# Optimization experiments

Hardware: AMD Instinct MI355X
Metric: run time of the kernel (lower is better)

Reference implementation:

```python
import jax, jax.numpy as jnp
import numpy as np

B, NP, NV, E = 256, 500, 50, 128
FP, FV = 16, 16
DEG_P, DEG_V = 6, 4


def setup_inputs() -> dict:
    key = jax.random.key(0)
    ks = jax.random.split(key, 16)
    rng = np.random.default_rng(0)

    def edges(nb, n, deg):
        per = deg * n
        off = np.repeat(np.arange(nb, dtype=np.int32) * n, per)
        ei = off[None, :] + rng.integers(0, n, size=(2, nb * per)).astype(np.int32)
        return jnp.asarray(ei)

    inp = {
        "p_x": jax.random.normal(ks[0], (B * NP, FP), jnp.float32),
        "v_x": jax.random.normal(ks[1], (B * NV, FV), jnp.float32),
        "p_edge_index": edges(B, NP, DEG_P),
        "v_edge_index": edges(B, NV, DEG_V),
        "p_batch": jnp.asarray(np.repeat(np.arange(B, dtype=np.int32), NP)),
        "v_batch": jnp.asarray(np.repeat(np.arange(B, dtype=np.int32), NV)),
    }

    def lin(k, fi, fo):
        s = 1.0 / np.sqrt(fi)
        kw, kb = jax.random.split(k)
        return (jax.random.uniform(kw, (fi, fo), jnp.float32, -s, s),
                jax.random.uniform(kb, (fo,), jnp.float32, -s, s))

    layers = [("pW0", "pb0", FP, E), ("pW1", "pb1", E, E), ("pW2", "pb2", E, E),
              ("vW0", "vb0", FV, E), ("vW1", "vb1", E, E), ("vW2", "vb2", E, E),
              ("hW1", "hb1", 4 * E, 2 * E), ("hW2", "hb2", 2 * E, E), ("hW3", "hb3", E, 1)]
    for j, (wn, bn, fi, fo) in enumerate(layers):
        W, b = lin(ks[2 + j], fi, fo)
        inp[wn] = W
        inp[bn] = b
    return inp


def _gcn(h, src, dst, dinv, W, b):
    # GCNConv: out[i] = sum_{j->i} dinv[j]*dinv[i] * (h[j] @ W) + dinv[i]^2 * (h[i] @ W) + b
    xw = h @ W
    msg = xw[src] * (dinv[src] * dinv[dst])[:, None]
    agg = jax.ops.segment_sum(msg, dst, num_segments=h.shape[0])
    return agg + xw * (dinv * dinv)[:, None] + b


def _encoder(x, edge_index, batch, W0, b0, W1, b1, W2, b2, nb, npg):
    N = x.shape[0]
    src, dst = edge_index[0], edge_index[1]
    h0 = x @ W0 + b0                                   # node_init_embeddings [N, E]
    ones_e = jnp.ones(src.shape[0], x.dtype)
    deg = 1.0 + jax.ops.segment_sum(ones_e, dst, num_segments=N)  # includes self loop
    dinv = jax.lax.rsqrt(deg)
    h = jax.nn.relu(_gcn(h0, src, dst, dinv, W1, b1))
    h = _gcn(h, src, dst, dinv, W2, b2)                # node_embeddings [N, E]
    counts = jax.ops.segment_sum(jnp.ones(N, x.dtype), batch, num_segments=nb)
    graph = jax.ops.segment_sum(h, batch, num_segments=nb) / counts[:, None]  # [nb, E]
    hd = h.reshape(nb, npg, -1)                        # to_dense_batch (equal-size graphs)
    h0d = h0.reshape(nb, npg, -1)
    gr = jnp.broadcast_to(graph[:, None, :], hd.shape)
    concat = jnp.concatenate([hd, h0d, gr], axis=-1)   # [nb, npg, 3E]
    mask = jnp.ones((nb, npg), bool)
    return graph, concat, mask


def reference(p_x, v_x, p_edge_index, v_edge_index, p_batch, v_batch,
              pW0, pb0, pW1, pb1, pW2, pb2,
              vW0, vb0, vW1, vb1, vW2, vb2,
              hW1, hb1, hW2, hb2, hW3, hb3):
    p_graph, _, _ = _encoder(p_x, p_edge_index, p_batch, pW0, pb0, pW1, pb1, pW2, pb2, B, NP)
    _, v_concat, v_mask = _encoder(v_x, v_edge_index, v_batch, vW0, vb0, vW1, vb1, vW2, vb2, B, NV)
    pg_rep = jnp.broadcast_to(p_graph[:, None, :], (B, NV, p_graph.shape[-1]))
    x = jnp.concatenate([v_concat, pg_rep], axis=-1)   # [B, NV, 4E]
    h = jax.nn.leaky_relu(x @ hW1 + hb1)
    h = jax.nn.leaky_relu(h @ hW2 + hb2)
    logits = (h @ hW3 + hb3)[..., 0]                   # [B, NV]
    return jnp.where(v_mask, logits, jnp.float32(-1e9))
```

## Files before the change

kernel.cpp:

```cpp
#include <hip/hip_runtime.h>
#include <hip/hip_bf16.h>

#define NP_TOT 128000
#define NV_TOT 12800
#define EP_EDGES 768000
#define EV_EDGES 51200
#define NB 256
#define PEPG 3000
#define VEPG 200
#define VCAP 24
#define PITCHV 138

typedef short bf16x8 __attribute__((ext_vector_type(8)));
typedef float f32x4 __attribute__((ext_vector_type(4)));

static __device__ __forceinline__ unsigned short f2bf(float f) {
    unsigned u = __builtin_bit_cast(unsigned, f);
    unsigned r = u + 0x7FFFu + ((u >> 16) & 1u);
    return (unsigned short)(r >> 16);
}
static __device__ __forceinline__ float bf2f(unsigned short h) {
    return __builtin_bit_cast(float, (unsigned)h << 16);
}

static __device__ __forceinline__ void frag_elem(const float* __restrict__ W,
                                                 short* __restrict__ Fh,
                                                 short* __restrict__ Fl,
                                                 int K, int M, int e) {
    if (e >= K * M) return;
    int col = e % M, kk = e / M;
    int ks = kk >> 5, rem = kk & 31, fq = rem >> 3, j = rem & 7;
    float v = W[(size_t)kk * M + col];
    unsigned short h = f2bf(v);
    size_t dst = (((size_t)col * (K >> 5) + ks) * 4 + fq) * 8 + j;
    Fh[dst] = (short)h;
    Fl[dst] = (short)f2bf(v - bf2f(h));
}

__global__ __launch_bounds__(256) void prep_k(
    const float* __restrict__ pW0, const float* __restrict__ pb0,
    const float* __restrict__ pW1,
    float* __restrict__ W01, float* __restrict__ b01,
    const float* __restrict__ vW1, short* __restrict__ W1vh, short* __restrict__ W1vl,
    const float* __restrict__ vW2, short* __restrict__ W2vh, short* __restrict__ W2vl,
    const float* __restrict__ hW1, short* __restrict__ H1h, short* __restrict__ H1l,
    const float* __restrict__ hW2, short* __restrict__ H2h, short* __restrict__ H2l) {
    int bid = blockIdx.x, t = threadIdx.x;
    if (bid == 0) {
        if (t < 128) {
            int col = t;
            float acc[17];
            #pragma unroll
            for (int r = 0; r < 17; r++) acc[r] = 0.f;
            for (int i = 0; i < 128; i++) {
                float w1 = pW1[i * 128 + col];
                #pragma unroll
                for (int r = 0; r < 16; r++) acc[r] += pW0[r * 128 + i] * w1;
                acc[16] += pb0[i] * w1;
            }
            #pragma unroll
            for (int r = 0; r < 16; r++) W01[r * 128 + col] = acc[r];
            b01[col] = acc[16];
        }
    } else if (bid < 65) {
        frag_elem(vW1, W1vh, W1vl, 128, 128, (bid - 1) * 256 + t);
    } else if (bid < 129) {
        frag_elem(vW2, W2vh, W2vl, 128, 128, (bid - 65) * 256 + t);
    } else if (bid < 641) {
        frag_elem(hW1, H1h, H1l, 512, 256, (bid - 129) * 256 + t);
    } else {
        frag_elem(hW2, H2h, H2l, 256, 128, (bid - 641) * 256 + t);
    }
}

__global__ __launch_bounds__(512) void pfused3(const float* __restrict__ x,
                                               const int* __restrict__ ei,
                                               const float* __restrict__ W01,
                                               const float* __restrict__ b01,
                                               const float* __restrict__ b1,
                                               float* __restrict__ p_gz) {
    __shared__ char lds[77824];
    float* sx = (float*)lds;
    unsigned short* sadj = (unsigned short*)(lds + 34816);
    char*  zb    = lds + 59392;
    float* sdinv = (float*)(lds + 69632);
    int*   scnt  = (int*)(lds + 71680);
    float* sbeta = (float*)(lds + 73728);
    float* scsum = (float*)(lds + 75776);

    const int t = threadIdx.x;
    const int b = blockIdx.x;

    scnt[t] = 0; scsum[t] = 0.f;
    const float4* x4 = (const float4*)(x + (size_t)b * 500 * 16);
    for (int i = t; i < 2000; i += 512) {
        float4 v = x4[i];
        int n = i >> 2, q = i & 3;
        float* dst = &sx[n * 17 + q * 4];
        dst[0] = v.x; dst[1] = v.y; dst[2] = v.z; dst[3] = v.w;
    }
    __syncthreads();

    const int* esrc = ei + (size_t)b * PEPG;
    const int* edst = ei + EP_EDGES + (size_t)b * PEPG;
    const int base = b * 500;

    for (int e = t; e < PEPG; e += 512) {
        int s = esrc[e] - base, d = edst[e] - base;
        int slot = atomicAdd(&scnt[d], 1);
        if (slot < VCAP) sadj[d * VCAP + slot] = (unsigned short)s;
    }
    __syncthreads();
    sdinv[t] = rsqrtf(1.0f + (float)scnt[t]);
    __syncthreads();

    for (int e = t; e < PEPG; e += 512)
        atomicAdd(&scsum[esrc[e] - base], sdinv[edst[e] - base]);
    __syncthreads();
    scsum[t] = (t < 500) ? sdinv[t] * (sdinv[t] + scsum[t]) * (1.0f / 500.0f) : 0.f;

    const int lane = t & 63;
    const int wvi = t >> 6;
    const int fr = lane & 15;
    const int fq = lane >> 4;
    const int col = wvi * 16 + fr;
    bf16x8 B1, B2;
    {
        float wt[8];
        #pragma unroll
        for (int j = 0; j < 8; j++)
            wt[j] = W01[(size_t)((fq * 8 + j) & 15) * 128 + col];
        short b1a[8], b2a[8];
        #pragma unroll
        for (int j = 0; j < 8; j++) {
            int kk = fq * 8 + j;
            unsigned short h = f2bf(wt[j]);
            b1a[j] = (short)h;
            b2a[j] = (kk < 16) ? (short)f2bf(wt[j] - bf2f(h)) : (short)0;
        }
        B1 = (bf16x8){b1a[0],b1a[1],b1a[2],b1a[3],b1a[4],b1a[5],b1a[6],b1a[7]};
        B2 = (bf16x8){b2a[0],b2a[1],b2a[2],b2a[3],b2a[4],b2a[5],b2a[6],b2a[7]};
    }
    float b01c = b01[col];
    float b1c = b1[col];
    float pools = 0.f;

    const int cg = t & 7, nb_ = t >> 3, c0 = cg * 2;
    #pragma unroll
    for (int ch = 0; ch < 4; ch++) {
        __syncthreads();
        #pragma unroll
        for (int pass = 0; pass < 2; pass++) {
            int n = ch * 128 + pass * 64 + nb_;
            char* zr = zb + (pass * 64 + nb_) * 80 + cg * 4;
            if (n < 500) {
                float di = sdinv[n];
                int d = scnt[n]; if (d > VCAP) d = VCAP;
                const unsigned short* ap = sadj + n * VCAP;
                float a0 = 0.f, a1 = 0.f, ts = 0.f;
                for (int e = 0; e < d; e++) {
                    int jl = ap[e];
                    float dj = sdinv[jl];
                    a0 += dj * sx[jl * 17 + c0];
                    a1 += dj * sx[jl * 17 + c0 + 1];
                    ts += dj;
                }
                float z0 = di * (di * sx[n * 17 + c0] + a0);
                float z1 = di * (di * sx[n * 17 + c0 + 1] + a1);
                unsigned short h0 = f2bf(z0), h1 = f2bf(z1);
                unsigned short l0 = f2bf(z0 - bf2f(h0)), l1 = f2bf(z1 - bf2f(h1));
                *(unsigned*)(zr)      = (unsigned)h0 | ((unsigned)h1 << 16);
                *(unsigned*)(zr + 32) = (unsigned)l0 | ((unsigned)l1 << 16);
                if (cg == 0) sbeta[n] = di * (di + ts);
            } else {
                *(unsigned*)(zr) = 0u;
                *(unsigned*)(zr + 32) = 0u;
                if (cg == 0) sbeta[n] = 0.f;
            }
        }
        __syncthreads();
        f32x4 acc[8];
        #pragma unroll
        for (int m = 0; m < 8; m++) acc[m] = (f32x4){0.f, 0.f, 0.f, 0.f};
        #pragma unroll
        for (int m = 0; m < 8; m++) {
            int rl = m * 16 + fr;
            bf16x8 a = *(bf16x8*)(zb + rl * 80 + fq * 16);
            acc[m] = __builtin_amdgcn_mfma_f32_16x16x32_bf16(a, B1, acc[m], 0, 0, 0);
            acc[m] = __builtin_amdgcn_mfma_f32_16x16x32_bf16(a, B2, acc[m], 0, 0, 0);
        }
        #pragma unroll
        for (int m = 0; m < 8; m++)
            #pragma unroll
            for (int j = 0; j < 4; j++) {
                int rl = ch * 128 + m * 16 + fq * 4 + j;
                float v = fmaxf(acc[m][j] + sbeta[rl] * b01c + b1c, 0.f);
                pools += scsum[rl] * v;
            }
    }
    pools += __shfl_xor(pools, 16);
    pools += __shfl_xor(pools, 32);
    if (fq == 0) p_gz[(size_t)b * 128 + col] = pools;
}

#define LB 0
#define LC 35328
#define LD 68096
#define LE 100864
#define E_SDINV (LE)
#define E_SCNT  (LE + 256)
#define E_SADJ  (LE + 512)
#define E_SVG   (LE + 5376)
#define E_VGH   (LE + 5888)
#define E_VGL   (LE + 6144)
#define E_PGH   (LE + 6400)
#define E_PGL   (LE + 6656)
#define E_WSUM  (LE + 6912)
__global__ __launch_bounds__(512) void vhead_k(
    const float* __restrict__ v_x,
    const int* __restrict__ v_ei,
    const float* __restrict__ W0, const float* __restrict__ b0,
    const short* __restrict__ W1h, const short* __restrict__ W1l,
    const float* __restrict__ b1,
    const short* __restrict__ W2h, const short* __restrict__ W2l,
    const float* __restrict__ b2,
    const float* __restrict__ p_gz,
    const float* __restrict__ pW2, const float* __restrict__ pb2,
    const short* __restrict__ H1h, const short* __restrict__ H1l,
    const float* __restrict__ hb1,
    const short* __restrict__ H2h, const short* __restrict__ H2l,
    const float* __restrict__ hb2,
    const float* __restrict__ w3, const float* __restrict__ b3,
    float* __restrict__ out) {
    __shared__ char lds[109824];
    const int t = threadIdx.x;
    const int b = blockIdx.x;
    const int lane = t & 63;
    const int wv = t >> 6;
    const int fr = lane & 15;
    const int fq = lane >> 4;
    float* Bf = (float*)(lds + LB);
    float* sdinv = (float*)(lds + E_SDINV);
    int*   scnt  = (int*)(lds + E_SCNT);
    int*   sadj  = (int*)(lds + E_SADJ);

    if (t < 64) scnt[t] = 0;
    *(float4*)(lds + LC + t * 16) = *((const float4*)W0 + t);
    {
        int col = t & 127, q = t >> 7;
        const float* gz = p_gz + (size_t)b * 128;
        float s = 0.f;
        #pragma unroll
        for (int k = 0; k < 32; k++)
            s += gz[q * 32 + k] * pW2[(size_t)(q * 32 + k) * 128 + col];
        ((float*)(lds + E_WSUM))[q * 128 + col] = s;
    }
    __syncthreads();

    if (t < VEPG) {
        int s = v_ei[b * VEPG + t] - b * 50;
        int d = v_ei[EV_EDGES + b * VEPG + t] - b * 50;
        int slot = atomicAdd(&scnt[d], 1);
        if (slot < VCAP) sadj[d * VCAP + slot] = s;
    }
    __syncthreads();

    if (t < 64)
        sdinv[t] = (t < 50) ? rsqrtf(1.0f + (float)scnt[t]) : 0.f;
    if (t < 128) {
        float* part = (float*)(lds + E_WSUM);
        float v = part[t] + part[128 + t] + part[256 + t] + part[384 + t] + pb2[t];
        unsigned short h = f2bf(v);
        ((short*)(lds + E_PGH))[t] = (short)h;
        ((short*)(lds + E_PGL))[t] = (short)f2bf(v - bf2f(h));
    }
    {
        int n = t >> 3, cg = t & 7;
        if (n < 50) {
            const float* sW0 = (const float*)(lds + LC);
            const float4* xr = (const float4*)(v_x + (size_t)(b * 50 + n) * 16);
            float4 x0 = xr[0], x1 = xr[1], x2 = xr[2], x3 = xr[3];
            float xv[16] = {x0.x,x0.y,x0.z,x0.w, x1.x,x1.y,x1.z,x1.w,
                            x2.x,x2.y,x2.z,x2.w, x3.x,x3.y,x3.z,x3.w};
            #pragma unroll
            for (int cc = 0; cc < 16; cc++) {
                int c = cg + cc * 8;
                float a = b0[c];
                #pragma unroll
                for (int k = 0; k < 16; k++) a += xv[k] * sW0[k * 128 + c];
                Bf[n * PITCHV + c] = a;
            }
        }
    }
    __syncthreads();

    {
        #pragma unroll
        for (int g = 0; g < 8; g++) {
            int r = g * 8 + wv;
            float2 v = *(const float2*)&Bf[r * PITCHV + 2 * lane];
            unsigned short h0 = f2bf(v.x), h1 = f2bf(v.y);
            unsigned short l0 = f2bf(v.x - bf2f(h0)), l1 = f2bf(v.y - bf2f(h1));
            int q = (256 + 4 * lane) ^ ((r & 7) << 4);
            *(unsigned*)(lds + LC + r * 512 + q) = (unsigned)h0 | ((unsigned)h1 << 16);
            *(unsigned*)(lds + LD + r * 512 + q) = (unsigned)l0 | ((unsigned)l1 << 16);
        }
        for (int g = 0; g < 7; g++) {
            int n = g * 8 + wv;
            if (n < 50) {
                float di = sdinv[n];
                int d = scnt[n]; if (d > VCAP) d = VCAP;
                const int* ap = sadj + n * VCAP;
                float2 a = *(const float2*)&Bf[n * PITCHV + 2 * lane];
                a.x *= di; a.y *= di;
                for (int e = 0; e < d; e++) {
                    int jl = ap[e];
                    float dj = sdinv[jl];
                    float2 v = *(const float2*)&Bf[jl * PITCHV + 2 * lane];
                    a.x += dj * v.x; a.y += dj * v.y;
                }
                float z0 = di * a.x, z1 = di * a.y;
                unsigned short h0 = f2bf(z0), h1 = f2bf(z1);
                unsigned short l0 = f2bf(z0 - bf2f(h0)), l1 = f2bf(z1 - bf2f(h1));
                int q = (4 * lane) ^ ((n & 7) << 4);
                *(unsigned*)(lds + LC + n * 512 + q) = (unsigned)h0 | ((unsigned)h1 << 16);
                *(unsigned*)(lds + LD + n * 512 + q) = (unsigned)l0 | ((unsigned)l1 << 16);
            }
        }
    }
    __syncthreads();

    {
        const int col = wv * 16 + fr;
        bf16x8 bh[4], bl[4];
        #pragma unroll
        for (int ks = 0; ks < 4; ks++) {
            int base = ((col * 4 + ks) * 4 + fq) * 8;
            bh[ks] = *(const bf16x8*)&W1h[base];
            bl[ks] = *(const bf16x8*)&W1l[base];
        }
        f32x4 acc[4];
        #pragma unroll
        for (int m = 0; m < 4; m++) acc[m] = (f32x4){0.f,0.f,0.f,0.f};
        #pragma unroll
        for (int ks = 0; ks < 4; ks++) {
            int kb = ks * 64 + fq * 16;
            #pragma unroll
            for (int m = 0; m < 4; m++) {
                int r = m * 16 + fr;
                int off = r * 512 + (kb ^ ((r & 7) << 4));
                bf16x8 ah = *(bf16x8*)(lds + LC + off);
                bf16x8 al = *(bf16x8*)(lds + LD + off);
                acc[m] = __builtin_amdgcn_mfma_f32_16x16x32_bf16(ah, bh[ks], acc[m], 0, 0, 0);
                acc[m] = __builtin_amdgcn_mfma_f32_16x16x32_bf16(ah, bl[ks], acc[m], 0, 0, 0);
                acc[m] = __builtin_amdgcn_mfma_f32_16x16x32_bf16(al, bh[ks], acc[m], 0, 0, 0);
            }
        }
        float b1c = b1[col];
        #pragma unroll
        for (int m = 0; m < 4; m++)
            #pragma unroll
            for (int j = 0; j < 4; j++) {
                int row = m * 16 + fq * 4 + j;
                Bf[row * PITCHV + col] = fmaxf(acc[m][j] + b1c, 0.f);
            }
    }
    __syncthreads();

    {
        for (int g = 0; g < 7; g++) {
            int n = g * 8 + wv;
            if (n < 50) {
                float di = sdinv[n];
                int d = scnt[n]; if (d > VCAP) d = VCAP;
                const int* ap = sadj + n * VCAP;
                float2 a = *(const float2*)&Bf[n * PITCHV + 2 * lane];
                a.x *= di; a.y *= di;
                for (int e = 0; e < d; e++) {
                    int jl = ap[e];
                    float dj = sdinv[jl];
                    float2 v = *(const float2*)&Bf[jl * PITCHV + 2 * lane];
                    a.x += dj * v.x; a.y += dj * v.y;
                }
                float z0 = di * a.x, z1 = di * a.y;
                unsigned short h0 = f2bf(z0), h1 = f2bf(z1);
                unsigned short l0 = f2bf(z0 - bf2f(h0)), l1 = f2bf(z1 - bf2f(h1));
                int q = (4 * lane) ^ ((n & 7) << 4);
                *(unsigned*)(lds + LC + n * 512 + q) = (unsigned)h0 | ((unsigned)h1 << 16);
                *(unsigned*)(lds + LD + n * 512 + q) = (unsigned)l0 | ((unsigned)l1 << 16);
            }
        }
    }
    __syncthreads();

    float h2v[4][4];
    {
        const int col = wv * 16 + fr;
        bf16x8 bh[4], bl[4];
        #pragma unroll
        for (int ks = 0; ks < 4; ks++) {
            int base = ((col * 4 + ks) * 4 + fq) * 8;
            bh[ks] = *(const bf16x8*)&W2h[base];
            bl[ks] = *(const bf16x8*)&W2l[base];
        }
        f32x4 acc[4];
        #pragma unroll
        for (int m = 0; m < 4; m++) acc[m] = (f32x4){0.f,0.f,0.f,0.f};
        #pragma unroll
        for (int ks = 0; ks < 4; ks++) {
            int kb = ks * 64 + fq * 16;
            #pragma unroll
            for (int m = 0; m < 4; m++) {
                int r = m * 16 + fr;
                int off = r * 512 + (kb ^ ((r & 7) << 4));
                bf16x8 ah = *(bf16x8*)(lds + LC + off);
                bf16x8 al = *(bf16x8*)(lds + LD + off);
                acc[m] = __builtin_amdgcn_mfma_f32_16x16x32_bf16(ah, bh[ks], acc[m], 0, 0, 0);
                acc[m] = __builtin_amdgcn_mfma_f32_16x16x32_bf16(ah, bl[ks], acc[m], 0, 0, 0);
                acc[m] = __builtin_amdgcn_mfma_f32_16x16x32_bf16(al, bh[ks], acc[m], 0, 0, 0);
            }
        }
        float b2c = b2[col];
        #pragma unroll
        for (int m = 0; m < 4; m++)
            #pragma unroll
            for (int j = 0; j < 4; j++) h2v[m][j] = acc[m][j] + b2c;
    }
    __syncthreads();

    {
        const int col = wv * 16 + fr;
        float s = 0.f;
        #pragma unroll
        for (int m = 0; m < 4; m++)
            #pragma unroll
            for (int j = 0; j < 4; j++) {
                int row = m * 16 + fq * 4 + j;
                float v = h2v[m][j];
                unsigned short h = f2bf(v);
                unsigned short l = f2bf(v - bf2f(h));
                int q = (2 * col) ^ ((row & 7) << 4);
                *(short*)(lds + LC + row * 512 + q) = (short)h;
                *(short*)(lds + LD + row * 512 + q) = (short)l;
                if (row < 50) s += v;
            }
        s += __shfl_xor(s, 16); s += __shfl_xor(s, 32);
        if (fq == 0) ((float*)(lds + E_SVG))[col] = s * (1.0f / 50.0f);
    }
    __syncthreads();

    if (t < 128) {
        float v = ((float*)(lds + E_SVG))[t];
        unsigned short h = f2bf(v);
        ((short*)(lds + E_VGH))[t] = (short)h;
        ((short*)(lds + E_VGL))[t] = (short)f2bf(v - bf2f(h));
    }
    __syncthreads();

    f32x4 accT[4][2];
    #pragma unroll
    for (int m = 0; m < 4; m++)
        #pragma unroll
        for (int nf = 0; nf < 2; nf++) accT[m][nf] = (f32x4){0.f,0.f,0.f,0.f};
    {
        #pragma unroll
        for (int ks = 0; ks < 16; ks++) {
            bf16x8 bh[2], bl[2];
            #pragma unroll
            for (int nf = 0; nf < 2; nf++) {
                int col2 = wv * 32 + nf * 16 + fr;
                int base = ((col2 * 16 + ks) * 4 + fq) * 8;
                bh[nf] = *(const bf16x8*)&H1h[base];
                bl[nf] = *(const bf16x8*)&H1l[base];
            }
            if (ks < 8) {
                int kb = ks * 64 + fq * 16;
                #pragma unroll
                for (int m = 0; m < 4; m++) {
                    int r = m * 16 + fr;
                    int off = r * 512 + (kb ^ ((r & 7) << 4));
                    bf16x8 ah = *(bf16x8*)(lds + LC + off);
                    bf16x8 al = *(bf16x8*)(lds + LD + off);
                    #pragma unroll
                    for (int nf = 0; nf < 2; nf++) {
                        accT[m][nf] = __builtin_amdgcn_mfma_f32_16x16x32_bf16(ah, bh[nf], accT[m][nf], 0, 0, 0);
                        accT[m][nf] = __builtin_amdgcn_mfma_f32_16x16x32_bf16(ah, bl[nf], accT[m][nf], 0, 0, 0);
                        accT[m][nf] = __builtin_amdgcn_mfma_f32_16x16x32_bf16(al, bh[nf], accT[m][nf], 0, 0, 0);
                    }
                }
            } else {
                int boff = (ks < 12) ? (E_VGH + (ks - 8) * 64 + fq * 16)
                                     : (E_PGH + (ks - 12) * 64 + fq * 16);
                int loff = boff + 256;
                bf16x8 ah = *(bf16x8*)(lds + boff);
                bf16x8 al = *(bf16x8*)(lds + loff);
                #pragma unroll
                for (int m = 0; m < 4; m++)
                    #pragma unroll
                    for (int nf = 0; nf < 2; nf++) {
                        accT[m][nf] = __builtin_amdgcn_mfma_f32_16x16x32_bf16(ah, bh[nf], accT[m][nf], 0, 0, 0);
                        accT[m][nf] = __builtin_amdgcn_mfma_f32_16x16x32_bf16(ah, bl[nf], accT[m][nf], 0, 0, 0);
                        accT[m][nf] = __builtin_amdgcn_mfma_f32_16x16x32_bf16(al, bh[nf], accT[m][nf], 0, 0, 0);
                    }
            }
        }
    }
    __syncthreads();
    {
        #pragma unroll
        for (int nf = 0; nf < 2; nf++) {
            int col2 = wv * 32 + nf * 16 + fr;
            float hc = hb1[col2];
            #pragma unroll
            for (int m = 0; m < 4; m++)
                #pragma unroll
                for (int j = 0; j < 4; j++) {
                    int row = m * 16 + fq * 4 + j;
                    float v = accT[m][nf][j] + hc;
                    v = v > 0.f ? v : 0.01f * v;
                    unsigned short h = f2bf(v);
                    unsigned short l = f2bf(v - bf2f(h));
                    int q = (2 * col2) ^ ((row & 7) << 4);
                    *(short*)(lds + LC + row * 512 + q) = (short)h;
                    *(short*)(lds + LD + row * 512 + q) = (short)l;
                }
        }
    }
    __syncthreads();

    {
        const int col3 = wv * 16 + fr;
        f32x4 acc[4];
        #pragma unroll
        for (int m = 0; m < 4; m++) acc[m] = (f32x4){0.f,0.f,0.f,0.f};
        #pragma unroll
        for (int ks = 0; ks < 8; ks++) {
            int base = ((col3 * 8 + ks) * 4 + fq) * 8;
            bf16x8 bh = *(const bf16x8*)&H2h[base];
            bf16x8 bl = *(const bf16x8*)&H2l[base];
            int kb = ks * 64 + fq * 16;
            #pragma unroll
            for (int m = 0; m < 4; m++) {
                int r = m * 16 + fr;
                int off = r * 512 + (kb ^ ((r & 7) << 4));
                bf16x8 ah = *(bf16x8*)(lds + LC + off);
                bf16x8 al = *(bf16x8*)(lds + LD + off);
                acc[m] = __builtin_amdgcn_mfma_f32_16x16x32_bf16(ah, bh, acc[m], 0, 0, 0);
                acc[m] = __builtin_amdgcn_mfma_f32_16x16x32_bf16(ah, bl, acc[m], 0, 0, 0);
                acc[m] = __builtin_amdgcn_mfma_f32_16x16x32_bf16(al, bh, acc[m], 0, 0, 0);
            }
        }
        float hc = hb2[col3], wc = w3[col3];
        float p[4][4];
        #pragma unroll
        for (int m = 0; m < 4; m++)
            #pragma unroll
            for (int j = 0; j < 4; j++) {
                float v = acc[m][j] + hc;
                v = v > 0.f ? v : 0.01f * v;
                p[m][j] = v * wc;
            }
        #pragma unroll
        for (int m = 0; m < 4; m++)
            #pragma unroll
            for (int j = 0; j < 4; j++) {
                p[m][j] += __shfl_xor(p[m][j], 1);
                p[m][j] += __shfl_xor(p[m][j], 2);
                p[m][j] += __shfl_xor(p[m][j], 4);
                p[m][j] += __shfl_xor(p[m][j], 8);
            }
        if (fr == 0) {
            float* wsum = (float*)(lds + E_WSUM);
            #pragma unroll
            for (int m = 0; m < 4; m++)
                #pragma unroll
                for (int j = 0; j < 4; j++)
                    wsum[wv * 64 + m * 16 + fq * 4 + j] = p[m][j];
        }
    }
    __syncthreads();
    if (t < 50) {
        float* wsum = (float*)(lds + E_WSUM);
        float s = 0.f;
        #pragma unroll
        for (int w8 = 0; w8 < 8; w8++) s += wsum[w8 * 64 + t];
        out[b * 50 + t] = s + b3[0];
    }
}

extern "C" void kernel_launch(void* const* d_in, const int* in_sizes, int n_in,
                              void* d_out, int out_size, void* d_ws, size_t ws_size,
                              hipStream_t stream) {
    const float* p_x = (const float*)d_in[0];
    const float* v_x = (const float*)d_in[1];
    const int* p_ei = (const int*)d_in[2];
    const int* v_ei = (const int*)d_in[3];
    const float* pW0 = (const float*)d_in[6];  const float* pb0 = (const float*)d_in[7];
    const float* pW1 = (const float*)d_in[8];  const float* pb1 = (const float*)d_in[9];
    const float* pW2 = (const float*)d_in[10]; const float* pb2 = (const float*)d_in[11];
    const float* vW0 = (const float*)d_in[12]; const float* vb0 = (const float*)d_in[13];
    const float* vW1 = (const float*)d_in[14]; const float* vb1 = (const float*)d_in[15];
    const float* vW2 = (const float*)d_in[16]; const float* vb2 = (const float*)d_in[17];
    const float* hW1 = (const float*)d_in[18]; const float* hb1 = (const float*)d_in[19];
    const float* hW2 = (const float*)d_in[20]; const float* hb2 = (const float*)d_in[21];
    const float* hW3 = (const float*)d_in[22]; const float* hb3 = (const float*)d_in[23];

    char* w = (char*)d_ws;
    size_t off = 0;
    auto alloc = [&](size_t bytes) { char* p = w + off; off += (bytes + 255) & ~size_t(255); return p; };
    float* p_gz = (float*)alloc((size_t)NB * 128 * 4);
    float* W01  = (float*)alloc((size_t)16 * 128 * 4);
    float* b01  = (float*)alloc((size_t)128 * 4);
    short* W1vh = (short*)alloc((size_t)128 * 128 * 2);
    short* W1vl = (short*)alloc((size_t)128 * 128 * 2);
    short* W2vh = (short*)alloc((size_t)128 * 128 * 2);
    short* W2vl = (short*)alloc((size_t)128 * 128 * 2);
    short* H1h  = (short*)alloc((size_t)512 * 256 * 2);
    short* H1l  = (short*)alloc((size_t)512 * 256 * 2);
    short* H2h  = (short*)alloc((size_t)256 * 128 * 2);
    short* H2l  = (short*)alloc((size_t)256 * 128 * 2);

    prep_k<<<769, 256, 0, stream>>>(pW0, pb0, pW1, W01, b01,
                                    vW1, W1vh, W1vl, vW2, W2vh, W2vl,
                                    hW1, H1h, H1l, hW2, H2h, H2l);
    pfused3<<<NB, 512, 0, stream>>>(p_x, p_ei, W01, b01, pb1, p_gz);
    vhead_k<<<NB, 512, 0, stream>>>(v_x, v_ei,
                                    vW0, vb0, W1vh, W1vl, vb1, W2vh, W2vl, vb2,
                                    p_gz, pW2, pb2, H1h, H1l, hb1, H2h, H2l, hb2,
                                    hW3, hb3, (float*)d_out);
}
```

Before: 83.04 us.

## Merge p-encoder and v-encoder/head kernels into one warp-specialized kernel

Replaces the separate p-side pooling kernel and the v-side/head kernel with a single kernel. Each block's first four waves run the p-graph GCN and pooling while the other four waves run the v-graph GCN layers at the same time. The pooled p-graph vector stays in LDS instead of going through global memory. This removes one launch and the dependency between the two kernels and overlaps the two encoders. The cost is much larger LDS use per block (about 150KB), which limits occupancy to one block per CU, and each side now works with half the threads.

```diff
diff --git a/kernel.cpp b/kernel.cpp
--- a/kernel.cpp
+++ b/kernel.cpp
@@ -8,8 +8,8 @@
 #define NB 256
 #define PEPG 3000
 #define VEPG 200
+#define PCAP 24
 #define VCAP 24
-#define PITCHV 138
 
 typedef short bf16x8 __attribute__((ext_vector_type(8)));
 typedef float f32x4 __attribute__((ext_vector_type(4)));
@@ -73,387 +73,457 @@
     }
 }
 
-__global__ __launch_bounds__(512) void pfused3(const float* __restrict__ x,
-                                               const int* __restrict__ ei,
-                                               const float* __restrict__ W01,
-                                               const float* __restrict__ b01,
-                                               const float* __restrict__ b1,
-                                               float* __restrict__ p_gz) {
-    __shared__ char lds[77824];
-    float* sx = (float*)lds;
-    unsigned short* sadj = (unsigned short*)(lds + 34816);
-    char*  zb    = lds + 59392;
-    float* sdinv = (float*)(lds + 69632);
-    int*   scnt  = (int*)(lds + 71680);
-    float* sbeta = (float*)(lds + 73728);
-    float* scsum = (float*)(lds + 75776);
-
-    const int t = threadIdx.x;
-    const int b = blockIdx.x;
-
-    scnt[t] = 0; scsum[t] = 0.f;
-    const float4* x4 = (const float4*)(x + (size_t)b * 500 * 16);
-    for (int i = t; i < 2000; i += 512) {
-        float4 v = x4[i];
-        int n = i >> 2, q = i & 3;
-        float* dst = &sx[n * 17 + q * 4];
-        dst[0] = v.x; dst[1] = v.y; dst[2] = v.z; dst[3] = v.w;
-    }
-    __syncthreads();
-
-    const int* esrc = ei + (size_t)b * PEPG;
-    const int* edst = ei + EP_EDGES + (size_t)b * PEPG;
-    const int base = b * 500;
-
-    for (int e = t; e < PEPG; e += 512) {
-        int s = esrc[e] - base, d = edst[e] - base;
-        int slot = atomicAdd(&scnt[d], 1);
-        if (slot < VCAP) sadj[d * VCAP + slot] = (unsigned short)s;
-    }
-    __syncthreads();
-    sdinv[t] = rsqrtf(1.0f + (float)scnt[t]);
-    __syncthreads();
-
-    for (int e = t; e < PEPG; e += 512)
-        atomicAdd(&scsum[esrc[e] - base], sdinv[edst[e] - base]);
-    __syncthreads();
-    scsum[t] = (t < 500) ? sdinv[t] * (sdinv[t] + scsum[t]) * (1.0f / 500.0f) : 0.f;
-
-    const int lane = t & 63;
-    const int wvi = t >> 6;
-    const int fr = lane & 15;
-    const int fq = lane >> 4;
-    const int col = wvi * 16 + fr;
-    bf16x8 B1, B2;
-    {
-        float wt[8];
-        #pragma unroll
-        for (int j = 0; j < 8; j++)
-            wt[j] = W01[(size_t)((fq * 8 + j) & 15) * 128 + col];
-        short b1a[8], b2a[8];
-        #pragma unroll
-        for (int j = 0; j < 8; j++) {
-            int kk = fq * 8 + j;
-            unsigned short h = f2bf(wt[j]);
-            b1a[j] = (short)h;
-            b2a[j] = (kk < 16) ? (short)f2bf(wt[j] - bf2f(h)) : (short)0;
-        }
-        B1 = (bf16x8){b1a[0],b1a[1],b1a[2],b1a[3],b1a[4],b1a[5],b1a[6],b1a[7]};
-        B2 = (bf16x8){b2a[0],b2a[1],b2a[2],b2a[3],b2a[4],b2a[5],b2a[6],b2a[7]};
-    }
-    float b01c = b01[col];
-    float b1c = b1[col];
-    float pools = 0.f;
-
-    const int cg = t & 7, nb_ = t >> 3, c0 = cg * 2;
-    #pragma unroll
-    for (int ch = 0; ch < 4; ch++) {
-        __syncthreads();
-        #pragma unroll
-        for (int pass = 0; pass < 2; pass++) {
-            int n = ch * 128 + pass * 64 + nb_;
-            char* zr = zb + (pass * 64 + nb_) * 80 + cg * 4;
-            if (n < 500) {
-                float di = sdinv[n];
-                int d = scnt[n]; if (d > VCAP) d = VCAP;
-                const unsigned short* ap = sadj + n * VCAP;
-                float a0 = 0.f, a1 = 0.f, ts = 0.f;
-                for (int e = 0; e < d; e++) {
-                    int jl = ap[e];
-                    float dj = sdinv[jl];
-                    a0 += dj * sx[jl * 17 + c0];
-                    a1 += dj * sx[jl * 17 + c0 + 1];
-                    ts += dj;
-                }
-                float z0 = di * (di * sx[n * 17 + c0] + a0);
-                float z1 = di * (di * sx[n * 17 + c0 + 1] + a1);
-                unsigned short h0 = f2bf(z0), h1 = f2bf(z1);
-                unsigned short l0 = f2bf(z0 - bf2f(h0)), l1 = f2bf(z1 - bf2f(h1));
-                *(unsigned*)(zr)      = (unsigned)h0 | ((unsigned)h1 << 16);
-                *(unsigned*)(zr + 32) = (unsigned)l0 | ((unsigned)l1 << 16);
-                if (cg == 0) sbeta[n] = di * (di + ts);
-            } else {
-                *(unsigned*)(zr) = 0u;
-                *(unsigned*)(zr + 32) = 0u;
-                if (cg == 0) sbeta[n] = 0.f;
-            }
-        }
-        __syncthreads();
-        f32x4 acc[8];
-        #pragma unroll
-        for (int m = 0; m < 8; m++) acc[m] = (f32x4){0.f, 0.f, 0.f, 0.f};
-        #pragma unroll
-        for (int m = 0; m < 8; m++) {
-            int rl = m * 16 + fr;
-            bf16x8 a = *(bf16x8*)(zb + rl * 80 + fq * 16);
-            acc[m] = __builtin_amdgcn_mfma_f32_16x16x32_bf16(a, B1, acc[m], 0, 0, 0);
-            acc[m] = __builtin_amdgcn_mfma_f32_16x16x32_bf16(a, B2, acc[m], 0, 0, 0);
-        }
-        #pragma unroll
-        for (int m = 0; m < 8; m++)
-            #pragma unroll
-            for (int j = 0; j < 4; j++) {
-                int rl = ch * 128 + m * 16 + fq * 4 + j;
-                float v = fmaxf(acc[m][j] + sbeta[rl] * b01c + b1c, 0.f);
-                pools += scsum[rl] * v;
-            }
-    }
-    pools += __shfl_xor(pools, 16);
-    pools += __shfl_xor(pools, 32);
-    if (fq == 0) p_gz[(size_t)b * 128 + col] = pools;
-}
-
-#define LB 0
-#define LC 35328
-#define LD 68096
-#define LE 100864
-#define E_SDINV (LE)
-#define E_SCNT  (LE + 256)
-#define E_SADJ  (LE + 512)
-#define E_SVG   (LE + 5376)
-#define E_VGH   (LE + 5888)
-#define E_VGL   (LE + 6144)
-#define E_PGH   (LE + 6400)
-#define E_PGL   (LE + 6656)
-#define E_WSUM  (LE + 6912)
-__global__ __launch_bounds__(512) void vhead_k(
-    const float* __restrict__ v_x,
-    const int* __restrict__ v_ei,
-    const float* __restrict__ W0, const float* __restrict__ b0,
+#define PSX   0
+#define PADJ  34816
+#define PZB   59392
+#define PDINV 69632
+#define PCNT  71680
+#define PBETA 73728
+#define PCSUM 75776
+#define VLC   77824
+#define VLD   110592
+#define VM    143360
+#define VDINV (VM)
+#define VCNT  (VM + 256)
+#define VADJ  (VM + 512)
+#define VSVG  (VM + 5312)
+#define VGH   (VM + 7360)
+#define VGL   (VM + 7616)
+#define PGH   (VM + 7872)
+#define PGL   (VM + 8128)
+#define WSUM  (VM + 8384)
+#define PGZ   (VM + 10432)
+__global__ __launch_bounds__(512) void mega_k(
+    const float* __restrict__ p_x, const int* __restrict__ p_ei,
+    const float* __restrict__ v_x, const int* __restrict__ v_ei,
+    const float* __restrict__ W01, const float* __restrict__ b01,
+    const float* __restrict__ pb1,
+    const float* __restrict__ pW2, const float* __restrict__ pb2,
+    const float* __restrict__ vW0, const float* __restrict__ vb0,
     const short* __restrict__ W1h, const short* __restrict__ W1l,
-    const float* __restrict__ b1,
+    const float* __restrict__ vb1,
     const short* __restrict__ W2h, const short* __restrict__ W2l,
-    const float* __restrict__ b2,
-    const float* __restrict__ p_gz,
-    const float* __restrict__ pW2, const float* __restrict__ pb2,
+    const float* __restrict__ vb2,
     const short* __restrict__ H1h, const short* __restrict__ H1l,
     const float* __restrict__ hb1,
     const short* __restrict__ H2h, const short* __restrict__ H2l,
     const float* __restrict__ hb2,
     const float* __restrict__ w3, const float* __restrict__ b3,
     float* __restrict__ out) {
-    __shared__ char lds[109824];
+    __shared__ char lds[154304];
     const int t = threadIdx.x;
     const int b = blockIdx.x;
     const int lane = t & 63;
     const int wv = t >> 6;
     const int fr = lane & 15;
     const int fq = lane >> 4;
-    float* Bf = (float*)(lds + LB);
-    float* sdinv = (float*)(lds + E_SDINV);
-    int*   scnt  = (int*)(lds + E_SCNT);
-    int*   sadj  = (int*)(lds + E_SADJ);
-
-    if (t < 64) scnt[t] = 0;
-    *(float4*)(lds + LC + t * 16) = *((const float4*)W0 + t);
-    {
-        int col = t & 127, q = t >> 7;
-        const float* gz = p_gz + (size_t)b * 128;
-        float s = 0.f;
-        #pragma unroll
-        for (int k = 0; k < 32; k++)
-            s += gz[q * 32 + k] * pW2[(size_t)(q * 32 + k) * 128 + col];
-        ((float*)(lds + E_WSUM))[q * 128 + col] = s;
-    }
-    __syncthreads();
-
-    if (t < VEPG) {
-        int s = v_ei[b * VEPG + t] - b * 50;
-        int d = v_ei[EV_EDGES + b * VEPG + t] - b * 50;
-        int slot = atomicAdd(&scnt[d], 1);
-        if (slot < VCAP) sadj[d * VCAP + slot] = s;
-    }
-    __syncthreads();
-
-    if (t < 64)
-        sdinv[t] = (t < 50) ? rsqrtf(1.0f + (float)scnt[t]) : 0.f;
-    if (t < 128) {
-        float* part = (float*)(lds + E_WSUM);
-        float v = part[t] + part[128 + t] + part[256 + t] + part[384 + t] + pb2[t];
-        unsigned short h = f2bf(v);
-        ((short*)(lds + E_PGH))[t] = (short)h;
-        ((short*)(lds + E_PGL))[t] = (short)f2bf(v - bf2f(h));
-    }
-    {
-        int n = t >> 3, cg = t & 7;
+    const bool pside = wv < 4;
+    const int tp = t;
+    const int tv = t - 256;
+    const int wvV = wv - 4;
+
+    float* sx    = (float*)(lds + PSX);
+    unsigned short* padj = (unsigned short*)(lds + PADJ);
+    float* pdinv = (float*)(lds + PDINV);
+    int*   pcnt  = (int*)(lds + PCNT);
+    float* pbeta = (float*)(lds + PBETA);
+    float* pcsum = (float*)(lds + PCSUM);
+    float* vdinv = (float*)(lds + VDINV);
+    int*   vcnt  = (int*)(lds + VCNT);
+    int*   vadj  = (int*)(lds + VADJ);
+
+    f32x4 accL[4][2];
+    float h2v[4][2][4];
+    float z2x[13], z2y[13];
+    float pools0 = 0.f, pools1 = 0.f;
+    bf16x8 pB1a, pB2a, pB1b, pB2b;
+    float b01c0, b01c1, b1c0, b1c1;
+
+    if (pside) {
+        pcnt[tp] = 0; pcnt[tp + 256] = 0;
+        pcsum[tp] = 0.f; pcsum[tp + 256] = 0.f;
+        const float4* x4 = (const float4*)(p_x + (size_t)b * 500 * 16);
+        for (int i = tp; i < 2000; i += 256) {
+            float4 v = x4[i];
+            int n = i >> 2, q = i & 3;
+            float* dst = &sx[n * 17 + q * 4];
+            dst[0] = v.x; dst[1] = v.y; dst[2] = v.z; dst[3] = v.w;
+        }
+    } else {
+        if (tv < 64) vcnt[tv] = 0;
+    }
+    __syncthreads();
+
+    if (pside) {
+        const int* esrc = p_ei + (size_t)b * PEPG;
+        const int* edst = p_ei + EP_EDGES + (size_t)b * PEPG;
+        const int base = b * 500;
+        for (int e = tp; e < PEPG; e += 256) {
+            int s = esrc[e] - base, d = edst[e] - base;
+            int slot = atomicAdd(&pcnt[d], 1);
+            if (slot < PCAP) padj[d * PCAP + slot] = (unsigned short)s;
+        }
+    } else {
+        if (tv < VEPG) {
+            int s = v_ei[b * VEPG + tv] - b * 50;
+            int d = v_ei[EV_EDGES + b * VEPG + tv] - b * 50;
+            int slot = atomicAdd(&vcnt[d], 1);
+            if (slot < VCAP) vadj[d * VCAP + slot] = s;
+        }
+        int n = tv >> 2, q = tv & 3;
         if (n < 50) {
-            const float* sW0 = (const float*)(lds + LC);
             const float4* xr = (const float4*)(v_x + (size_t)(b * 50 + n) * 16);
             float4 x0 = xr[0], x1 = xr[1], x2 = xr[2], x3 = xr[3];
             float xv[16] = {x0.x,x0.y,x0.z,x0.w, x1.x,x1.y,x1.z,x1.w,
                             x2.x,x2.y,x2.z,x2.w, x3.x,x3.y,x3.z,x3.w};
             #pragma unroll
-            for (int cc = 0; cc < 16; cc++) {
-                int c = cg + cc * 8;
-                float a = b0[c];
-                #pragma unroll
-                for (int k = 0; k < 16; k++) a += xv[k] * sW0[k * 128 + c];
-                Bf[n * PITCHV + c] = a;
-            }
-        }
-    }
-    __syncthreads();
-
-    {
-        #pragma unroll
-        for (int g = 0; g < 8; g++) {
-            int r = g * 8 + wv;
-            float2 v = *(const float2*)&Bf[r * PITCHV + 2 * lane];
-            unsigned short h0 = f2bf(v.x), h1 = f2bf(v.y);
-            unsigned short l0 = f2bf(v.x - bf2f(h0)), l1 = f2bf(v.y - bf2f(h1));
-            int q = (256 + 4 * lane) ^ ((r & 7) << 4);
-            *(unsigned*)(lds + LC + r * 512 + q) = (unsigned)h0 | ((unsigned)h1 << 16);
-            *(unsigned*)(lds + LD + r * 512 + q) = (unsigned)l0 | ((unsigned)l1 << 16);
-        }
-        for (int g = 0; g < 7; g++) {
-            int n = g * 8 + wv;
+            for (int cc = 0; cc < 32; cc += 2) {
+                int c = q * 32 + cc;
+                float a0 = vb0[c], a1 = vb0[c + 1];
+                #pragma unroll
+                for (int k = 0; k < 16; k++) {
+                    a0 += xv[k] * vW0[k * 128 + c];
+                    a1 += xv[k] * vW0[k * 128 + c + 1];
+                }
+                unsigned short h0 = f2bf(a0), h1 = f2bf(a1);
+                unsigned short l0 = f2bf(a0 - bf2f(h0)), l1 = f2bf(a1 - bf2f(h1));
+                int qb = (256 + 2 * c) ^ ((n & 7) << 4);
+                *(unsigned*)(lds + VLC + n * 512 + qb) = (unsigned)h0 | ((unsigned)h1 << 16);
+                *(unsigned*)(lds + VLD + n * 512 + qb) = (unsigned)l0 | ((unsigned)l1 << 16);
+            }
+        }
+    }
+    __syncthreads();
+
+    if (pside) {
+        pdinv[tp] = rsqrtf(1.0f + (float)pcnt[tp]);
+        pdinv[tp + 256] = rsqrtf(1.0f + (float)pcnt[tp + 256]);
+    } else {
+        if (tv < 64) vdinv[tv] = (tv < 50) ? rsqrtf(1.0f + (float)vcnt[tv]) : 0.f;
+    }
+    __syncthreads();
+
+    if (pside) {
+        const int* esrc = p_ei + (size_t)b * PEPG;
+        const int* edst = p_ei + EP_EDGES + (size_t)b * PEPG;
+        const int base = b * 500;
+        for (int e = tp; e < PEPG; e += 256)
+            atomicAdd(&pcsum[esrc[e] - base], pdinv[edst[e] - base]);
+    } else {
+        for (int g = 0; g < 13; g++) {
+            int n = g * 4 + wvV;
             if (n < 50) {
-                float di = sdinv[n];
-                int d = scnt[n]; if (d > VCAP) d = VCAP;
-                const int* ap = sadj + n * VCAP;
-                float2 a = *(const float2*)&Bf[n * PITCHV + 2 * lane];
-                a.x *= di; a.y *= di;
+                float di = vdinv[n];
+                int d = vcnt[n]; if (d > VCAP) d = VCAP;
+                const int* ap = vadj + n * VCAP;
+                int qb = (256 + 4 * lane) ^ ((n & 7) << 4);
+                unsigned hw = *(unsigned*)(lds + VLC + n * 512 + qb);
+                unsigned lw = *(unsigned*)(lds + VLD + n * 512 + qb);
+                float ax = (bf2f((unsigned short)hw) + bf2f((unsigned short)lw)) * di;
+                float ay = (bf2f((unsigned short)(hw >> 16)) + bf2f((unsigned short)(lw >> 16))) * di;
                 for (int e = 0; e < d; e++) {
                     int jl = ap[e];
-                    float dj = sdinv[jl];
-                    float2 v = *(const float2*)&Bf[jl * PITCHV + 2 * lane];
-                    a.x += dj * v.x; a.y += dj * v.y;
-                }
-                float z0 = di * a.x, z1 = di * a.y;
+                    float dj = vdinv[jl];
+                    int qj = (256 + 4 * lane) ^ ((jl & 7) << 4);
+                    unsigned hj = *(unsigned*)(lds + VLC + jl * 512 + qj);
+                    unsigned lj = *(unsigned*)(lds + VLD + jl * 512 + qj);
+                    ax += dj * (bf2f((unsigned short)hj) + bf2f((unsigned short)lj));
+                    ay += dj * (bf2f((unsigned short)(hj >> 16)) + bf2f((unsigned short)(lj >> 16)));
+                }
+                float z0 = di * ax, z1 = di * ay;
                 unsigned short h0 = f2bf(z0), h1 = f2bf(z1);
                 unsigned short l0 = f2bf(z0 - bf2f(h0)), l1 = f2bf(z1 - bf2f(h1));
-                int q = (4 * lane) ^ ((n & 7) << 4);
-                *(unsigned*)(lds + LC + n * 512 + q) = (unsigned)h0 | ((unsigned)h1 << 16);
-                *(unsigned*)(lds + LD + n * 512 + q) = (unsigned)l0 | ((unsigned)l1 << 16);
-            }
-        }
-    }
-    __syncthreads();
-
-    {
-        const int col = wv * 16 + fr;
-        bf16x8 bh[4], bl[4];
+                int qo = (4 * lane) ^ ((n & 7) << 4);
+                *(unsigned*)(lds + VLC + n * 512 + qo) = (unsigned)h0 | ((unsigned)h1 << 16);
+                *(unsigned*)(lds + VLD + n * 512 + qo) = (unsigned)l0 | ((unsigned)l1 << 16);
+            }
+        }
+    }
+    __syncthreads();
+
+    if (pside) {
+        #pragma unroll
+        for (int rep = 0; rep < 2; rep++) {
+            int idx = tp + rep * 256;
+            pcsum[idx] = (idx < 500) ? pdinv[idx] * (pdinv[idx] + pcsum[idx]) * (1.0f / 500.0f) : 0.f;
+        }
+        int col0 = wv * 16 + fr;
+        float wt0[8], wt1[8];
+        #pragma unroll
+        for (int j = 0; j < 8; j++) {
+            wt0[j] = W01[(size_t)((fq * 8 + j) & 15) * 128 + col0];
+            wt1[j] = W01[(size_t)((fq * 8 + j) & 15) * 128 + col0 + 64];
+        }
+        short a1[8], a2[8], c1[8], c2[8];
+        #pragma unroll
+        for (int j = 0; j < 8; j++) {
+            int kk = fq * 8 + j;
+            unsigned short h0 = f2bf(wt0[j]);
+            unsigned short h1 = f2bf(wt1[j]);
+            a1[j] = (short)h0;
+            c1[j] = (short)h1;
+            a2[j] = (kk < 16) ? (short)f2bf(wt0[j] - bf2f(h0)) : (short)0;
+            c2[j] = (kk < 16) ? (short)f2bf(wt1[j] - bf2f(h1)) : (short)0;
+        }
+        pB1a = (bf16x8){a1[0],a1[1],a1[2],a1[3],a1[4],a1[5],a1[6],a1[7]};
+        pB2a = (bf16x8){a2[0],a2[1],a2[2],a2[3],a2[4],a2[5],a2[6],a2[7]};
+        pB1b = (bf16x8){c1[0],c1[1],c1[2],c1[3],c1[4],c1[5],c1[6],c1[7]};
+        pB2b = (bf16x8){c2[0],c2[1],c2[2],c2[3],c2[4],c2[5],c2[6],c2[7]};
+        b01c0 = b01[col0]; b01c1 = b01[col0 + 64];
+        b1c0 = pb1[col0];  b1c1 = pb1[col0 + 64];
+    } else {
+        #pragma unroll
+        for (int m = 0; m < 4; m++)
+            #pragma unroll
+            for (int cg = 0; cg < 2; cg++) accL[m][cg] = (f32x4){0.f,0.f,0.f,0.f};
         #pragma unroll
         for (int ks = 0; ks < 4; ks++) {
-            int base = ((col * 4 + ks) * 4 + fq) * 8;
-            bh[ks] = *(const bf16x8*)&W1h[base];
-            bl[ks] = *(const bf16x8*)&W1l[base];
-        }
-        f32x4 acc[4];
-        #pragma unroll
-        for (int m = 0; m < 4; m++) acc[m] = (f32x4){0.f,0.f,0.f,0.f};
-        #pragma unroll
-        for (int ks = 0; ks < 4; ks++) {
+            bf16x8 bh[2], bl[2];
+            #pragma unroll
+            for (int cg = 0; cg < 2; cg++) {
+                int col = cg * 64 + wvV * 16 + fr;
+                int base = ((col * 4 + ks) * 4 + fq) * 8;
+                bh[cg] = *(const bf16x8*)&W1h[base];
+                bl[cg] = *(const bf16x8*)&W1l[base];
+            }
             int kb = ks * 64 + fq * 16;
             #pragma unroll
             for (int m = 0; m < 4; m++) {
                 int r = m * 16 + fr;
                 int off = r * 512 + (kb ^ ((r & 7) << 4));
-                bf16x8 ah = *(bf16x8*)(lds + LC + off);
-                bf16x8 al = *(bf16x8*)(lds + LD + off);
-                acc[m] = __builtin_amdgcn_mfma_f32_16x16x32_bf16(ah, bh[ks], acc[m], 0, 0, 0);
-                acc[m] = __builtin_amdgcn_mfma_f32_16x16x32_bf16(ah, bl[ks], acc[m], 0, 0, 0);
-                acc[m] = __builtin_amdgcn_mfma_f32_16x16x32_bf16(al, bh[ks], acc[m], 0, 0, 0);
-            }
-        }
-        float b1c = b1[col];
-        #pragma unroll
-        for (int m = 0; m < 4; m++)
-            #pragma unroll
-            for (int j = 0; j < 4; j++) {
-                int row = m * 16 + fq * 4 + j;
-                Bf[row * PITCHV + col] = fmaxf(acc[m][j] + b1c, 0.f);
-            }
+                bf16x8 ah = *(bf16x8*)(lds + VLC + off);
+                bf16x8 al = *(bf16x8*)(lds + VLD + off);
+                #pragma unroll
+                for (int cg = 0; cg < 2; cg++) {
+                    accL[m][cg] = __builtin_amdgcn_mfma_f32_16x16x32_bf16(ah, bh[cg], accL[m][cg], 0, 0, 0);
+                    accL[m][cg] = __builtin_amdgcn_mfma_f32_16x16x32_bf16(ah, bl[cg], accL[m][cg], 0, 0, 0);
+                    accL[m][cg] = __builtin_amdgcn_mfma_f32_16x16x32_bf16(al, bh[cg], accL[m][cg], 0, 0, 0);
+                }
+            }
+        }
+    }
+    __syncthreads();
+
+    #pragma unroll
+    for (int ch = 0; ch < 4; ch++) {
+        if (pside) {
+            int cg = tp & 7, nb_ = tp >> 3, c0 = cg * 2;
+            #pragma unroll
+            for (int pass = 0; pass < 4; pass++) {
+                int nloc = pass * 32 + nb_;
+                int n = ch * 128 + nloc;
+                char* zr = lds + PZB + nloc * 80 + cg * 4;
+                if (n < 500) {
+                    float di = pdinv[n];
+                    int d = pcnt[n]; if (d > PCAP) d = PCAP;
+                    const unsigned short* ap = padj + n * PCAP;
+                    float a0 = 0.f, a1 = 0.f, ts = 0.f;
+                    for (int e = 0; e < d; e++) {
+                        int jl = ap[e];
+                        float dj = pdinv[jl];
+                        a0 += dj * sx[jl * 17 + c0];
+                        a1 += dj * sx[jl * 17 + c0 + 1];
+                        ts += dj;
+                    }
+                    float z0 = di * (di * sx[n * 17 + c0] + a0);
+                    float z1 = di * (di * sx[n * 17 + c0 + 1] + a1);
+                    unsigned short h0 = f2bf(z0), h1 = f2bf(z1);
+                    unsigned short l0 = f2bf(z0 - bf2f(h0)), l1 = f2bf(z1 - bf2f(h1));
+                    *(unsigned*)(zr)      = (unsigned)h0 | ((unsigned)h1 << 16);
+                    *(unsigned*)(zr + 32) = (unsigned)l0 | ((unsigned)l1 << 16);
+                    if (cg == 0) pbeta[n] = di * (di + ts);
+                } else {
+                    *(unsigned*)(zr) = 0u;
+                    *(unsigned*)(zr + 32) = 0u;
+                    if (cg == 0) pbeta[n] = 0.f;
+                }
+            }
+        } else {
+            if (ch == 0) {
+                #pragma unroll
+                for (int cg = 0; cg < 2; cg++) {
+                    int col = cg * 64 + wvV * 16 + fr;
+                    float bc = vb1[col];
+                    #pragma unroll
+                    for (int m = 0; m < 4; m++)
+                        #pragma unroll
+                        for (int j = 0; j < 4; j++) {
+                            int row = m * 16 + fq * 4 + j;
+                            float v = fmaxf(accL[m][cg][j] + bc, 0.f);
+                            unsigned short h = f2bf(v);
+                            unsigned short l = f2bf(v - bf2f(h));
+                            int qb = (2 * col) ^ ((row & 7) << 4);
+                            *(short*)(lds + VLC + row * 512 + qb) = (short)h;
+                            *(short*)(lds + VLD + row * 512 + qb) = (short)l;
+                        }
+                }
+            } else if (ch == 1) {
+                for (int g = 0; g < 13; g++) {
+                    int n = g * 4 + wvV;
+                    z2x[g] = 0.f; z2y[g] = 0.f;
+                    if (n < 50) {
+                        float di = vdinv[n];
+                        int d = vcnt[n]; if (d > VCAP) d = VCAP;
+                        const int* ap = vadj + n * VCAP;
+                        int qb = (4 * lane) ^ ((n & 7) << 4);
+                        unsigned hw = *(unsigned*)(lds + VLC + n * 512 + qb);
+                        unsigned lw = *(unsigned*)(lds + VLD + n * 512 + qb);
+                        float ax = (bf2f((unsigned short)hw) + bf2f((unsigned short)lw)) * di;
+                        float ay = (bf2f((unsigned short)(hw >> 16)) + bf2f((unsigned short)(lw >> 16))) * di;
+                        for (int e = 0; e < d; e++) {
+                            int jl = ap[e];
+                            float dj = vdinv[jl];
+                            int qj = (4 * lane) ^ ((jl & 7) << 4);
+                            unsigned hj = *(unsigned*)(lds + VLC + jl * 512 + qj);
+                            unsigned lj = *(unsigned*)(lds + VLD + jl * 512 + qj);
+                            ax += dj * (bf2f((unsigned short)hj) + bf2f((unsigned short)lj));
+                            ay += dj * (bf2f((unsigned short)(hj >> 16)) + bf2f((unsigned short)(lj >> 16)));
+                        }
+                        z2x[g] = di * ax; z2y[g] = di * ay;
+                    }
+                }
+            } else if (ch == 2) {
+                for (int g = 0; g < 13; g++) {
+                    int n = g * 4 + wvV;
+                    if (n < 50) {
+                        unsigned short h0 = f2bf(z2x[g]), h1 = f2bf(z2y[g]);
+                        unsigned short l0 = f2bf(z2x[g] - bf2f(h0)), l1 = f2bf(z2y[g] - bf2f(h1));
+                        int qo = (4 * lane) ^ ((n & 7) << 4);
+                        *(unsigned*)(lds + VLC + n * 512 + qo) = (unsigned)h0 | ((unsigned)h1 << 16);
+                        *(unsigned*)(lds + VLD + n * 512 + qo) = (unsigned)l0 | ((unsigned)l1 << 16);
+                    }
+                }
+            }
+        }
+        __syncthreads();
+
+        if (pside) {
+            f32x4 acc0[8], acc1[8];
+            #pragma unroll
+            for (int m = 0; m < 8; m++) {
+                acc0[m] = (f32x4){0.f,0.f,0.f,0.f};
+                acc1[m] = (f32x4){0.f,0.f,0.f,0.f};
+            }
+            #pragma unroll
+            for (int m = 0; m < 8; m++) {
+                int rlz = m * 16 + fr;
+                bf16x8 a = *(bf16x8*)(lds + PZB + rlz * 80 + fq * 16);
+                acc0[m] = __builtin_amdgcn_mfma_f32_16x16x32_bf16(a, pB1a, acc0[m], 0, 0, 0);
+                acc0[m] = __builtin_amdgcn_mfma_f32_16x16x32_bf16(a, pB2a, acc0[m], 0, 0, 0);
+                acc1[m] = __builtin_amdgcn_mfma_f32_16x16x32_bf16(a, pB1b, acc1[m], 0, 0, 0);
+                acc1[m] = __builtin_amdgcn_mfma_f32_16x16x32_bf16(a, pB2b, acc1[m], 0, 0, 0);
+            }
+            #pragma unroll
+            for (int m = 0; m < 8; m++)
+                #pragma unroll
+                for (int j = 0; j < 4; j++) {
+                    int rl = ch * 128 + m * 16 + fq * 4 + j;
+                    float v0 = fmaxf(acc0[m][j] + pbeta[rl] * b01c0 + b1c0, 0.f);
+                    float v1 = fmaxf(acc1[m][j] + pbeta[rl] * b01c1 + b1c1, 0.f);
+                    pools0 += pcsum[rl] * v0;
+                    pools1 += pcsum[rl] * v1;
+                }
+        } else {
+            if (ch == 1) {
+            } else if (ch == 2) {
+                #pragma unroll
+                for (int m = 0; m < 4; m++)
+                    #pragma unroll
+                    for (int cg = 0; cg < 2; cg++) accL[m][cg] = (f32x4){0.f,0.f,0.f,0.f};
+                #pragma unroll
+                for (int ks = 0; ks < 4; ks++) {
+                    bf16x8 bh[2], bl[2];
+                    #pragma unroll
+                    for (int cg = 0; cg < 2; cg++) {
+                        int col = cg * 64 + wvV * 16 + fr;
+                        int base = ((col * 4 + ks) * 4 + fq) * 8;
+                        bh[cg] = *(const bf16x8*)&W2h[base];
+                        bl[cg] = *(const bf16x8*)&W2l[base];
+                    }
+                    int kb = ks * 64 + fq * 16;
+                    #pragma unroll
+                    for (int m = 0; m < 4; m++) {
+                        int r = m * 16 + fr;
+                        int off = r * 512 + (kb ^ ((r & 7) << 4));
+                        bf16x8 ah = *(bf16x8*)(lds + VLC + off);
+                        bf16x8 al = *(bf16x8*)(lds + VLD + off);
+                        #pragma unroll
+                        for (int cg = 0; cg < 2; cg++) {
+                            accL[m][cg] = __builtin_amdgcn_mfma_f32_16x16x32_bf16(ah, bh[cg], accL[m][cg], 0, 0, 0);
+                            accL[m][cg] = __builtin_amdgcn_mfma_f32_16x16x32_bf16(ah, bl[cg], accL[m][cg], 0, 0, 0);
+                            accL[m][cg] = __builtin_amdgcn_mfma_f32_16x16x32_bf16(al, bh[cg], accL[m][cg], 0, 0, 0);
+                        }
+                    }
+                }
+                #pragma unroll
+                for (int m = 0; m < 4; m++)
+                    #pragma unroll
+                    for (int cg = 0; cg < 2; cg++) {
+                        int col = cg * 64 + wvV * 16 + fr;
+                        float bc = vb2[col];
+                        #pragma unroll
+                        for (int j = 0; j < 4; j++) h2v[m][cg][j] = accL[m][cg][j] + bc;
+                    }
+            } else if (ch == 3) {
+                #pragma unroll
+                for (int cg = 0; cg < 2; cg++) {
+                    int col = cg * 64 + wvV * 16 + fr;
+                    float s = 0.f;
+                    #pragma unroll
+                    for (int m = 0; m < 4; m++)
+                        #pragma unroll
+                        for (int j = 0; j < 4; j++) {
+                            int row = m * 16 + fq * 4 + j;
+                            float v = h2v[m][cg][j];
+                            unsigned short h = f2bf(v);
+                            unsigned short l = f2bf(v - bf2f(h));
+                            int qb = (2 * col) ^ ((row & 7) << 4);
+                            *(short*)(lds + VLC + row * 512 + qb) = (short)h;
+                            *(short*)(lds + VLD + row * 512 + qb) = (short)l;
+                            if (row < 50) s += v;
+                        }
+                    s += __shfl_xor(s, 16); s += __shfl_xor(s, 32);
+                    if (fq == 0) ((float*)(lds + VSVG))[wvV * 128 + col] = s;
+                }
+            }
+        }
+        __syncthreads();
+    }
+
+    if (pside) {
+        pools0 += __shfl_xor(pools0, 16); pools0 += __shfl_xor(pools0, 32);
+        pools1 += __shfl_xor(pools1, 16); pools1 += __shfl_xor(pools1, 32);
+        if (fq == 0) {
+            int col0 = wv * 16 + fr;
+            ((float*)(lds + PGZ))[col0] = pools0;
+            ((float*)(lds + PGZ))[col0 + 64] = pools1;
+        }
+    } else {
+        if (tv < 128) {
+            float* svg = (float*)(lds + VSVG);
+            float v = (svg[tv] + svg[128 + tv] + svg[256 + tv] + svg[384 + tv]) * (1.0f / 50.0f);
+            unsigned short h = f2bf(v);
+            ((short*)(lds + VGH))[tv] = (short)h;
+            ((short*)(lds + VGL))[tv] = (short)f2bf(v - bf2f(h));
+        }
     }
     __syncthreads();
 
     {
-        for (int g = 0; g < 7; g++) {
-            int n = g * 8 + wv;
-            if (n < 50) {
-                float di = sdinv[n];
-                int d = scnt[n]; if (d > VCAP) d = VCAP;
-                const int* ap = sadj + n * VCAP;
-                float2 a = *(const float2*)&Bf[n * PITCHV + 2 * lane];
-                a.x *= di; a.y *= di;
-                for (int e = 0; e < d; e++) {
-                    int jl = ap[e];
-                    float dj = sdinv[jl];
-                    float2 v = *(const float2*)&Bf[jl * PITCHV + 2 * lane];
-                    a.x += dj * v.x; a.y += dj * v.y;
-                }
-                float z0 = di * a.x, z1 = di * a.y;
-                unsigned short h0 = f2bf(z0), h1 = f2bf(z1);
-                unsigned short l0 = f2bf(z0 - bf2f(h0)), l1 = f2bf(z1 - bf2f(h1));
-                int q = (4 * lane) ^ ((n & 7) << 4);
-                *(unsigned*)(lds + LC + n * 512 + q) = (unsigned)h0 | ((unsigned)h1 << 16);
-                *(unsigned*)(lds + LD + n * 512 + q) = (unsigned)l0 | ((unsigned)l1 << 16);
-            }
-        }
-    }
-    __syncthreads();
-
-    float h2v[4][4];
-    {
-        const int col = wv * 16 + fr;
-        bf16x8 bh[4], bl[4];
-        #pragma unroll
-        for (int ks = 0; ks < 4; ks++) {
-            int base = ((col * 4 + ks) * 4 + fq) * 8;
-            bh[ks] = *(const bf16x8*)&W2h[base];
-            bl[ks] = *(const bf16x8*)&W2l[base];
-        }
-        f32x4 acc[4];
-        #pragma unroll
-        for (int m = 0; m < 4; m++) acc[m] = (f32x4){0.f,0.f,0.f,0.f};
-        #pragma unroll
-        for (int ks = 0; ks < 4; ks++) {
-            int kb = ks * 64 + fq * 16;
-            #pragma unroll
-            for (int m = 0; m < 4; m++) {
-                int r = m * 16 + fr;
-                int off = r * 512 + (kb ^ ((r & 7) << 4));
-                bf16x8 ah = *(bf16x8*)(lds + LC + off);
-                bf16x8 al = *(bf16x8*)(lds + LD + off);
-                acc[m] = __builtin_amdgcn_mfma_f32_16x16x32_bf16(ah, bh[ks], acc[m], 0, 0, 0);
-                acc[m] = __builtin_amdgcn_mfma_f32_16x16x32_bf16(ah, bl[ks], acc[m], 0, 0, 0);
-                acc[m] = __builtin_amdgcn_mfma_f32_16x16x32_bf16(al, bh[ks], acc[m], 0, 0, 0);
-            }
-        }
-        float b2c = b2[col];
-        #pragma unroll
-        for (int m = 0; m < 4; m++)
-            #pragma unroll
-            for (int j = 0; j < 4; j++) h2v[m][j] = acc[m][j] + b2c;
-    }
-    __syncthreads();
-
-    {
-        const int col = wv * 16 + fr;
+        int col = t & 127, q = t >> 7;
+        const float* gz = (const float*)(lds + PGZ);
         float s = 0.f;
         #pragma unroll
-        for (int m = 0; m < 4; m++)
-            #pragma unroll
-            for (int j = 0; j < 4; j++) {
-                int row = m * 16 + fq * 4 + j;
-                float v = h2v[m][j];
-                unsigned short h = f2bf(v);
-                unsigned short l = f2bf(v - bf2f(h));
-                int q = (2 * col) ^ ((row & 7) << 4);
-                *(short*)(lds + LC + row * 512 + q) = (short)h;
-                *(short*)(lds + LD + row * 512 + q) = (short)l;
-                if (row < 50) s += v;
-            }
-        s += __shfl_xor(s, 16); s += __shfl_xor(s, 32);
-        if (fq == 0) ((float*)(lds + E_SVG))[col] = s * (1.0f / 50.0f);
-    }
-    __syncthreads();
-
+        for (int k = 0; k < 32; k++)
+            s += gz[q * 32 + k] * pW2[(size_t)(q * 32 + k) * 128 + col];
+        sx[q * 128 + col] = s;
+    }
+    __syncthreads();
     if (t < 128) {
-        float v = ((float*)(lds + E_SVG))[t];
+        float v = sx[t] + sx[128 + t] + sx[256 + t] + sx[384 + t] + pb2[t];
         unsigned short h = f2bf(v);
-        ((short*)(lds + E_VGH))[t] = (short)h;
-        ((short*)(lds + E_VGL))[t] = (short)f2bf(v - bf2f(h));
+        ((short*)(lds + PGH))[t] = (short)h;
+        ((short*)(lds + PGL))[t] = (short)f2bf(v - bf2f(h));
     }
     __syncthreads();
 
@@ -479,8 +549,8 @@
                 for (int m = 0; m < 4; m++) {
                     int r = m * 16 + fr;
                     int off = r * 512 + (kb ^ ((r & 7) << 4));
-                    bf16x8 ah = *(bf16x8*)(lds + LC + off);
-                    bf16x8 al = *(bf16x8*)(lds + LD + off);
+                    bf16x8 ah = *(bf16x8*)(lds + VLC + off);
+                    bf16x8 al = *(bf16x8*)(lds + VLD + off);
                     #pragma unroll
                     for (int nf = 0; nf < 2; nf++) {
                         accT[m][nf] = __builtin_amdgcn_mfma_f32_16x16x32_bf16(ah, bh[nf], accT[m][nf], 0, 0, 0);
@@ -489,8 +559,8 @@
                     }
                 }
             } else {
-                int boff = (ks < 12) ? (E_VGH + (ks - 8) * 64 + fq * 16)
-                                     : (E_PGH + (ks - 12) * 64 + fq * 16);
+                int boff = (ks < 12) ? (VGH + (ks - 8) * 64 + fq * 16)
+                                     : (PGH + (ks - 12) * 64 + fq * 16);
                 int loff = boff + 256;
                 bf16x8 ah = *(bf16x8*)(lds + boff);
                 bf16x8 al = *(bf16x8*)(lds + loff);
@@ -520,9 +590,9 @@
                     v = v > 0.f ? v : 0.01f * v;
                     unsigned short h = f2bf(v);
                     unsigned short l = f2bf(v - bf2f(h));
-                    int q = (2 * col2) ^ ((row & 7) << 4);
-                    *(short*)(lds + LC + row * 512 + q) = (short)h;
-                    *(short*)(lds + LD + row * 512 + q) = (short)l;
+                    int qb = (2 * col2) ^ ((row & 7) << 4);
+                    *(short*)(lds + VLC + row * 512 + qb) = (short)h;
+                    *(short*)(lds + VLD + row * 512 + qb) = (short)l;
                 }
         }
     }
@@ -543,8 +613,8 @@
             for (int m = 0; m < 4; m++) {
                 int r = m * 16 + fr;
                 int off = r * 512 + (kb ^ ((r & 7) << 4));
-                bf16x8 ah = *(bf16x8*)(lds + LC + off);
-                bf16x8 al = *(bf16x8*)(lds + LD + off);
+                bf16x8 ah = *(bf16x8*)(lds + VLC + off);
+                bf16x8 al = *(bf16x8*)(lds + VLD + off);
                 acc[m] = __builtin_amdgcn_mfma_f32_16x16x32_bf16(ah, bh, acc[m], 0, 0, 0);
                 acc[m] = __builtin_amdgcn_mfma_f32_16x16x32_bf16(ah, bl, acc[m], 0, 0, 0);
                 acc[m] = __builtin_amdgcn_mfma_f32_16x16x32_bf16(al, bh, acc[m], 0, 0, 0);
@@ -570,7 +640,7 @@
                 p[m][j] += __shfl_xor(p[m][j], 8);
             }
         if (fr == 0) {
-            float* wsum = (float*)(lds + E_WSUM);
+            float* wsum = (float*)(lds + WSUM);
             #pragma unroll
             for (int m = 0; m < 4; m++)
                 #pragma unroll
@@ -580,7 +650,7 @@
     }
     __syncthreads();
     if (t < 50) {
-        float* wsum = (float*)(lds + E_WSUM);
+        float* wsum = (float*)(lds + WSUM);
         float s = 0.f;
         #pragma unroll
         for (int w8 = 0; w8 < 8; w8++) s += wsum[w8 * 64 + t];
@@ -608,7 +678,6 @@
     char* w = (char*)d_ws;
     size_t off = 0;
     auto alloc = [&](size_t bytes) { char* p = w + off; off += (bytes + 255) & ~size_t(255); return p; };
-    float* p_gz = (float*)alloc((size_t)NB * 128 * 4);
     float* W01  = (float*)alloc((size_t)16 * 128 * 4);
     float* b01  = (float*)alloc((size_t)128 * 4);
     short* W1vh = (short*)alloc((size_t)128 * 128 * 2);
@@ -623,9 +692,9 @@
     prep_k<<<769, 256, 0, stream>>>(pW0, pb0, pW1, W01, b01,
                                     vW1, W1vh, W1vl, vW2, W2vh, W2vl,
                                     hW1, H1h, H1l, hW2, H2h, H2l);
-    pfused3<<<NB, 512, 0, stream>>>(p_x, p_ei, W01, b01, pb1, p_gz);
-    vhead_k<<<NB, 512, 0, stream>>>(v_x, v_ei,
-                                    vW0, vb0, W1vh, W1vl, vb1, W2vh, W2vl, vb2,
-                                    p_gz, pW2, pb2, H1h, H1l, hb1, H2h, H2l, hb2,
-                                    hW3, hb3, (float*)d_out);
+    mega_k<<<NB, 512, 0, stream>>>(p_x, p_ei, v_x, v_ei,
+                                   W01, b01, pb1, pW2, pb2,
+                                   vW0, vb0, W1vh, W1vl, vb1, W2vh, W2vl, vb2,
+                                   H1h, H1l, hb1, H2h, H2l, hb2,
+                                   hW3, hb3, (float*)d_out);
 }
```

Result: slower. 148.5 us (+78.9%).
